# Optimization experiments

Hardware: AMD Instinct MI355X
Metric: run time of the kernel (lower is better)

## Reference

```python
import jax, jax.numpy as jnp
import numpy as np

NX = 41                      # cube side: 2*r_max/voxel + 1 with r_max=6.0, voxel=0.3
VOXEL = 0.3
R_MAX = 6.0
MIN_DIST = 0.8
MIN_SEP = max(1, int(round(MIN_DIST / VOXEL)))   # 3 voxels
K = 4                        # topk_per_channel
NEG = -1.0e9                 # fp32 sentinel used by the torch module
VALID_THRESH = -1.0e8


def setup_inputs() -> dict:
    key = jax.random.key(0)
    B, N, C = 1, 128, 4
    G = NX ** 3
    ax = np.arange(NX)
    ii, jj, kk = np.meshgrid(ax, ax, ax, indexing='ij')
    coords = np.stack([ii, jj, kk], axis=-1).reshape(-1, 3)          # [G,3] integer voxel coords
    center = (NX - 1) / 2.0
    grid_xyz = ((coords - center) * VOXEL).astype(np.float32)        # [G,3] local Angstrom coords
    sphere_mask = np.linalg.norm(grid_xyz, axis=-1) <= R_MAX         # [G] bool
    k1, k2, k3 = jax.random.split(key, 3)
    density = jax.random.normal(k1, (B, N, C, G), jnp.float32)
    A = jax.random.normal(k2, (B, N, 3, 3), jnp.float32)
    Rmats, _ = jnp.linalg.qr(A)                                      # proper-ish rotation matrices
    tpos = jax.random.normal(k3, (B, N, 3), jnp.float32)
    node_mask = jnp.ones((B, N), jnp.float32)
    return dict(density=density,
                grid_xyz=jnp.asarray(grid_xyz),
                sphere_mask=jnp.asarray(sphere_mask),
                coords_int=jnp.asarray(coords, jnp.int32),
                Rmats=Rmats, tpos=tpos, node_mask=node_mask)


def extract_peaks(density, grid_xyz, sphere_mask, coords_int):
    # density: [B,N,C,G]; iterative argmax peak-picking with Chebyshev NMS suppression.
    v0 = jnp.where(sphere_mask[None, None, None, :], density, NEG)
    cx = coords_int[:, 0][None, None, None, :]   # [1,1,1,G]
    cy = coords_int[:, 1][None, None, None, :]
    cz = coords_int[:, 2][None, None, None, :]

    def step(v, _):
        idx = jnp.argmax(v, axis=-1)                                   # [B,N,C]
        score = jnp.take_along_axis(v, idx[..., None], axis=-1)[..., 0]
        valid = score > VALID_THRESH
        xyz = grid_xyz[idx]                                            # [B,N,C,3]
        ijk = coords_int[idx]                                          # [B,N,C,3]
        # Chebyshev (max-abs) voxel distance to the picked peak, per axis to avoid a [.,G,3] temp
        d = jnp.maximum(jnp.maximum(jnp.abs(cx - ijk[..., 0:1]),
                                    jnp.abs(cy - ijk[..., 1:2])),
                        jnp.abs(cz - ijk[..., 2:3]))                    # [B,N,C,G]
        suppress = (d <= MIN_SEP) & valid[..., None]
        v = jnp.where(suppress, NEG, v)
        out = (jnp.where(valid, score, NEG),
               jnp.where(valid[..., None], xyz, 0.0),
               valid)
        return v, out

    _, (scores, xyz, mask) = jax.lax.scan(step, v0, None, length=K)
    # K is leading scan axis -> move to axis 3 giving [B,N,C,K,...]
    return (jnp.moveaxis(xyz, 0, 3), jnp.moveaxis(scores, 0, 3), jnp.moveaxis(mask, 0, 3))


def reference(density, grid_xyz, sphere_mask, coords_int, Rmats, tpos, node_mask):
    peaks_xyz, peaks_score, peaks_mask = extract_peaks(density, grid_xyz, sphere_mask, coords_int)
    # local -> global frame: R @ x + t
    coords_global = jnp.einsum('bnij,bnckj->bncki', Rmats, peaks_xyz) + tpos[:, :, None, None, :]
    m = node_mask[..., None, None, None]                                # [B,N,1,1,1]
    coords_local = peaks_xyz * m
    coords_global = coords_global * m
    scores = peaks_score * node_mask[..., None, None]
    mask = peaks_mask & node_mask.astype(bool)[..., None, None]
    return coords_local, coords_global, scores, mask
```

## Files before the change

kernel.cpp:

```cpp
#include <hip/hip_runtime.h>

#define G_VOX  68921
#define GMAX   68920
#define NSEG   272
#define MWORDS 2176
#define NEGV (-1.0e9f)
#define VTH  (-1.0e8f)

__device__ __forceinline__ bool sphere_bit(const float* __restrict__ gxyz, int e) {
    if (e >= G_VOX) return false;
    float gx = gxyz[e * 3 + 0];
    float gy = gxyz[e * 3 + 1];
    float gz = gxyz[e * 3 + 2];
    float s  = __fadd_rn(__fadd_rn(__fmul_rn(gx, gx), __fmul_rn(gy, gy)),
                         __fmul_rn(gz, gz));
    return (__fsqrt_rn(s) <= 6.0f);
}

__global__ __launch_bounds__(256) void build_mask(
    const float* __restrict__ gxyz, unsigned int* __restrict__ mask)
{
    int idx = blockIdx.x * 256 + threadIdx.x;
    unsigned long long bal = __ballot(sphere_bit(gxyz, idx));
    int lane = threadIdx.x & 63;
    if (lane == 0)       mask[idx >> 5] = (unsigned int)bal;
    else if (lane == 32) mask[idx >> 5] = (unsigned int)(bal >> 32);
}

__device__ __forceinline__ void seg_scan8_core(
    const float* __restrict__ dens, const unsigned int* smw,
    int ebase, int sh, int eclamp, float& bv, int& bi)
{
    bv = NEGV; bi = ebase;
    float4       dq[8];
    unsigned int bq[8];
    unsigned int wprev = smw[0];
    #pragma unroll
    for (int q = 0; q < 8; ++q) {
        const int e = ebase + 32 * q;
        const unsigned int wnext = smw[q + 1];
        unsigned long long mw = ((unsigned long long)wnext << 32) | wprev;
        bq[q] = (unsigned int)(mw >> sh) & 0xFu;
        wprev = wnext;
        const int ec = (e + 3 <= GMAX) ? e : eclamp;
        if (bq[q]) dq[q] = *reinterpret_cast<const float4*>(dens + ec);
    }
    #pragma unroll
    for (int q = 0; q < 8; ++q) {
        if (bq[q]) {
            const int e = ebase + 32 * q;
            float v0 = (bq[q] & 1u) ? dq[q].x : NEGV;
            float v1 = (bq[q] & 2u) ? dq[q].y : NEGV;
            float v2 = (bq[q] & 4u) ? dq[q].z : NEGV;
            float v3 = (bq[q] & 8u) ? dq[q].w : NEGV;
            if (v0 > bv) { bv = v0; bi = e;     }
            if (v1 > bv) { bv = v1; bi = e + 1; }
            if (v2 > bv) { bv = v2; bi = e + 2; }
            if (v3 > bv) { bv = v3; bi = e + 3; }
        }
    }
    #pragma unroll
    for (int off = 4; off > 0; off >>= 1) {
        float ov = __shfl_xor(bv, off);
        int   oi = __shfl_xor(bi, off);
        if (ov > bv || (ov == bv && oi < bi)) { bv = ov; bi = oi; }
    }
}

__global__ __launch_bounds__(512) void fused_peaks(
    const float* __restrict__ density,
    const float* __restrict__ gxyz,
    const unsigned int* __restrict__ maskg,
    const float* __restrict__ Rm, const float* __restrict__ tp,
    const float* __restrict__ nmask,
    float* __restrict__ out)
{
    __shared__ unsigned int smask[MWORDS + 2];
    __shared__ float sval[NSEG];
    __shared__ int   sidx[NSEG];
    __shared__ int   flag[NSEG];
    __shared__ int   list[104];
    __shared__ int   nlist;
    __shared__ float rv[8];
    __shared__ int   ri[8];
    __shared__ float pval[4];
    __shared__ int   pidx[4];
    __shared__ int   pki[4], pkj[4], pkk[4];

    const int tid  = threadIdx.x;
    const int nc   = blockIdx.x;
    const int n    = nc >> 2;
    const int h    = (-nc) & 3;
    const int lane = tid & 63;
    const int w    = tid >> 6;
    const int s8   = lane >> 3;
    const int l8   = lane & 7;
    const float* dens = density + (size_t)nc * G_VOX;
    const int eclamp = h + ((GMAX - 3 - h) & ~3);

    for (int i = tid; i < MWORDS + 2; i += 512) smask[i] = (i < MWORDS) ? maskg[i] : 0u;
    for (int i = tid; i < NSEG; i += 512) flag[i] = 0;
    __syncthreads();

    for (int g = w; g < 34; g += 8) {
        const int s = g * 8 + s8;
        const int ebase = h + 256 * s + 4 * l8;
        float bv; int bi;
        seg_scan8_core(dens, smask + 8 * s, ebase, h + 4 * l8, eclamp, bv, bi);
        if (l8 == 0) { sval[s] = bv; sidx[s] = bi; }
    }
    __syncthreads();

    for (int p = 0; p < 4; ++p) {
        float bv = -INFINITY;
        int   bi = 0x7FFFFFFF;
        if (tid < NSEG) { bv = sval[tid]; bi = sidx[tid]; }
        #pragma unroll
        for (int off = 32; off > 0; off >>= 1) {
            float ov = __shfl_down(bv, off);
            int   oi = __shfl_down(bi, off);
            if (ov > bv || (ov == bv && oi < bi)) { bv = ov; bi = oi; }
        }
        if (lane == 0) { rv[w] = bv; ri[w] = bi; }
        __syncthreads();
        if (w == 0) {
            bv = (lane < 8) ? rv[lane] : -INFINITY;
            bi = (lane < 8) ? ri[lane] : 0x7FFFFFFF;
            #pragma unroll
            for (int off = 4; off > 0; off >>= 1) {
                float ov = __shfl_down(bv, off);
                int   oi = __shfl_down(bi, off);
                if (ov > bv || (ov == bv && oi < bi)) { bv = ov; bi = oi; }
            }
            if (lane == 0) {
                pval[p] = bv;
                pidx[p] = bi;
                int pi = bi / 1681;
                int rr = bi - pi * 1681;
                int pj = rr / 41;
                pki[p] = pi; pkj[p] = pj; pkk[p] = rr - pj * 41;
                nlist = 0;
            }
        }
        __syncthreads();

        if (p < 3 && pval[p] > VTH) {
            if (tid < 49) {
                int di = tid / 7 - 3, dj = tid % 7 - 3;
                int ii = pki[p] + di, jj = pkj[p] + dj;
                if (ii >= 0 && ii <= 40 && jj >= 0 && jj <= 40) {
                    int k0 = pkk[p] - 3; if (k0 < 0)  k0 = 0;
                    int k1 = pkk[p] + 3; if (k1 > 40) k1 = 40;
                    int b0  = ii * 1681 + jj * 41 + k0;
                    int cnt = k1 - k0 + 1;
                    unsigned long long m = ((1ull << cnt) - 1ull) << (b0 & 31);
                    int w0 = b0 >> 5;
                    atomicAnd(&smask[w0], ~(unsigned int)m);
                    unsigned int hi = (unsigned int)(m >> 32);
                    if (hi) atomicAnd(&smask[w0 + 1], ~hi);
                    int s0 = (b0 > h) ? (b0 - h) >> 8 : 0;
                    int s1 = (b0 + cnt - 1 > h) ? (b0 + cnt - 1 - h) >> 8 : 0;
                    #pragma unroll
                    for (int t2 = 0; t2 < 2; ++t2) {
                        const int s = t2 ? s1 : s0;
                        if (t2 && s1 == s0) break;
                        int widx = sidx[s];
                        int wi = widx / 1681;
                        int wr = widx - wi * 1681;
                        int wj = wr / 41;
                        int wk = wr - wj * 41;
                        int ci = wi - pki[p]; if (ci < 0) ci = -ci;
                        int cj = wj - pkj[p]; if (cj < 0) cj = -cj;
                        int ck = wk - pkk[p]; if (ck < 0) ck = -ck;
                        if (ci <= 3 && cj <= 3 && ck <= 3) {
                            if (atomicMax(&flag[s], p + 1) < p + 1) {
                                int q = atomicAdd(&nlist, 1); list[q] = s;
                            }
                        }
                    }
                }
            }
            __syncthreads();
            const int cnt = nlist;
            for (int base = 0; base < cnt; base += 64) {
                const int slot = base + w * 8 + s8;
                if (slot < cnt) {
                    const int s = list[slot];
                    const int ebase = h + 256 * s + 4 * l8;
                    float bv2; int bi2;
                    seg_scan8_core(dens, smask + 8 * s, ebase, h + 4 * l8, eclamp, bv2, bi2);
                    if (l8 == 0) { sval[s] = bv2; sidx[s] = bi2; }
                }
            }
        }
        __syncthreads();
    }

    if (tid < 4) {
        const int k   = tid;
        const float val = pval[k];
        const int   idx = pidx[k];
        const bool valid = val > VTH;
        float gx = 0.0f, gy = 0.0f, gz = 0.0f;
        if (valid) {
            gx = gxyz[idx * 3 + 0];
            gy = gxyz[idx * 3 + 1];
            gz = gxyz[idx * 3 + 2];
        }
        const float nm = nmask[n];
        const float* R = Rm + n * 9;
        const float* t = tp + n * 3;
        float wx = R[0] * gx + R[1] * gy + R[2] * gz + t[0];
        float wy = R[3] * gx + R[4] * gy + R[5] * gz + t[1];
        float wz = R[6] * gx + R[7] * gy + R[8] * gz + t[2];

        const size_t o3 = ((size_t)nc * 4 + k) * 3;
        out[o3 + 0] = gx * nm;
        out[o3 + 1] = gy * nm;
        out[o3 + 2] = gz * nm;
        out[6144 + o3 + 0] = wx * nm;
        out[6144 + o3 + 1] = wy * nm;
        out[6144 + o3 + 2] = wz * nm;
        const size_t o1 = (size_t)nc * 4 + k;
        out[12288 + o1] = (valid ? val : NEGV) * nm;
        out[14336 + o1] = (valid && nm != 0.0f) ? 1.0f : 0.0f;
    }
}

extern "C" void kernel_launch(void* const* d_in, const int* in_sizes, int n_in,
                              void* d_out, int out_size, void* d_ws, size_t ws_size,
                              hipStream_t stream) {
    const float* density  = (const float*)d_in[0];
    const float* grid_xyz = (const float*)d_in[1];
    const float* Rm    = (const float*)d_in[4];
    const float* tpos  = (const float*)d_in[5];
    const float* nmask = (const float*)d_in[6];
    float* out = (float*)d_out;

    unsigned int* mask = (unsigned int*)d_ws;

    build_mask<<<dim3(272), dim3(256), 0, stream>>>(grid_xyz, mask);
    fused_peaks<<<dim3(512), dim3(512), 0, stream>>>(density, grid_xyz, mask,
                                                     Rm, tpos, nmask, out);
}
```

Before: 221.9 us.

## Run iterative peak-pick and NMS rescans in a single wavefront without block barriers

After the initial full segment scan, the four peak-pick iterations (argmax reduction, mask suppression, and rescans of affected segments) now run entirely in wavefront 0. Block-wide __syncthreads and the cross-wave shared-memory reduction are dropped in favour of wave-level shuffles. The aim is to cut barrier and reduction latency in the serial tail. In exchange, the rescans of affected segments use 8 lanes-groups of one wave instead of all 8 waves, so rescan throughput drops. Correctness also now depends on lockstep execution within the wave for the LDS atomics and the list reads.

Result: no change. 218.7 us (-1.4%).

```diff
diff --git a/kernel.cpp b/kernel.cpp
--- a/kernel.cpp
+++ b/kernel.cpp
@@ -81,11 +81,8 @@
     __shared__ int   flag[NSEG];
     __shared__ int   list[104];
     __shared__ int   nlist;
-    __shared__ float rv[8];
-    __shared__ int   ri[8];
     __shared__ float pval[4];
     __shared__ int   pidx[4];
-    __shared__ int   pki[4], pkj[4], pkk[4];
 
     const int tid  = threadIdx.x;
     const int nc   = blockIdx.x;
@@ -111,119 +108,107 @@
     }
     __syncthreads();
 
-    for (int p = 0; p < 4; ++p) {
-        float bv = -INFINITY;
-        int   bi = 0x7FFFFFFF;
-        if (tid < NSEG) { bv = sval[tid]; bi = sidx[tid]; }
-        #pragma unroll
-        for (int off = 32; off > 0; off >>= 1) {
-            float ov = __shfl_down(bv, off);
-            int   oi = __shfl_down(bi, off);
-            if (ov > bv || (ov == bv && oi < bi)) { bv = ov; bi = oi; }
-        }
-        if (lane == 0) { rv[w] = bv; ri[w] = bi; }
-        __syncthreads();
-        if (w == 0) {
-            bv = (lane < 8) ? rv[lane] : -INFINITY;
-            bi = (lane < 8) ? ri[lane] : 0x7FFFFFFF;
+    if (w == 0) {
+        for (int p = 0; p < 4; ++p) {
+            float bv = -INFINITY;
+            int   bi = 0x7FFFFFFF;
+            for (int t = lane; t < NSEG; t += 64) {
+                float v = sval[t]; int ix = sidx[t];
+                if (v > bv || (v == bv && ix < bi)) { bv = v; bi = ix; }
+            }
             #pragma unroll
-            for (int off = 4; off > 0; off >>= 1) {
+            for (int off = 32; off > 0; off >>= 1) {
                 float ov = __shfl_down(bv, off);
                 int   oi = __shfl_down(bi, off);
                 if (ov > bv || (ov == bv && oi < bi)) { bv = ov; bi = oi; }
             }
-            if (lane == 0) {
-                pval[p] = bv;
-                pidx[p] = bi;
-                int pi = bi / 1681;
-                int rr = bi - pi * 1681;
-                int pj = rr / 41;
-                pki[p] = pi; pkj[p] = pj; pkk[p] = rr - pj * 41;
-                nlist = 0;
-            }
-        }
-        __syncthreads();
-
-        if (p < 3 && pval[p] > VTH) {
-            if (tid < 49) {
-                int di = tid / 7 - 3, dj = tid % 7 - 3;
-                int ii = pki[p] + di, jj = pkj[p] + dj;
-                if (ii >= 0 && ii <= 40 && jj >= 0 && jj <= 40) {
-                    int k0 = pkk[p] - 3; if (k0 < 0)  k0 = 0;
-                    int k1 = pkk[p] + 3; if (k1 > 40) k1 = 40;
-                    int b0  = ii * 1681 + jj * 41 + k0;
-                    int cnt = k1 - k0 + 1;
-                    unsigned long long m = ((1ull << cnt) - 1ull) << (b0 & 31);
-                    int w0 = b0 >> 5;
-                    atomicAnd(&smask[w0], ~(unsigned int)m);
-                    unsigned int hi = (unsigned int)(m >> 32);
-                    if (hi) atomicAnd(&smask[w0 + 1], ~hi);
-                    int s0 = (b0 > h) ? (b0 - h) >> 8 : 0;
-                    int s1 = (b0 + cnt - 1 > h) ? (b0 + cnt - 1 - h) >> 8 : 0;
-                    #pragma unroll
-                    for (int t2 = 0; t2 < 2; ++t2) {
-                        const int s = t2 ? s1 : s0;
-                        if (t2 && s1 == s0) break;
-                        int widx = sidx[s];
-                        int wi = widx / 1681;
-                        int wr = widx - wi * 1681;
-                        int wj = wr / 41;
-                        int wk = wr - wj * 41;
-                        int ci = wi - pki[p]; if (ci < 0) ci = -ci;
-                        int cj = wj - pkj[p]; if (cj < 0) cj = -cj;
-                        int ck = wk - pkk[p]; if (ck < 0) ck = -ck;
-                        if (ci <= 3 && cj <= 3 && ck <= 3) {
-                            if (atomicMax(&flag[s], p + 1) < p + 1) {
-                                int q = atomicAdd(&nlist, 1); list[q] = s;
+            const float pv = __shfl(bv, 0);
+            const int   px = __shfl(bi, 0);
+            if (lane == 0) { pval[p] = pv; pidx[p] = px; nlist = 0; }
+            const int pi = px / 1681;
+            const int rr = px - pi * 1681;
+            const int pj = rr / 41;
+            const int pk = rr - pj * 41;
+
+            if (p < 3 && pv > VTH) {
+                if (lane < 49) {
+                    int di = lane / 7 - 3, dj = lane % 7 - 3;
+                    int ii = pi + di, jj = pj + dj;
+                    if (ii >= 0 && ii <= 40 && jj >= 0 && jj <= 40) {
+                        int k0 = pk - 3; if (k0 < 0)  k0 = 0;
+                        int k1 = pk + 3; if (k1 > 40) k1 = 40;
+                        int b0  = ii * 1681 + jj * 41 + k0;
+                        int cnt = k1 - k0 + 1;
+                        unsigned long long m = ((1ull << cnt) - 1ull) << (b0 & 31);
+                        int w0 = b0 >> 5;
+                        atomicAnd(&smask[w0], ~(unsigned int)m);
+                        unsigned int hi = (unsigned int)(m >> 32);
+                        if (hi) atomicAnd(&smask[w0 + 1], ~hi);
+                        int s0 = (b0 > h) ? (b0 - h) >> 8 : 0;
+                        int s1 = (b0 + cnt - 1 > h) ? (b0 + cnt - 1 - h) >> 8 : 0;
+                        #pragma unroll
+                        for (int t2 = 0; t2 < 2; ++t2) {
+                            const int s = t2 ? s1 : s0;
+                            if (t2 && s1 == s0) break;
+                            int widx = sidx[s];
+                            int wi = widx / 1681;
+                            int wr = widx - wi * 1681;
+                            int wj = wr / 41;
+                            int wk = wr - wj * 41;
+                            int ci = wi - pi; if (ci < 0) ci = -ci;
+                            int cj = wj - pj; if (cj < 0) cj = -cj;
+                            int ck = wk - pk; if (ck < 0) ck = -ck;
+                            if (ci <= 3 && cj <= 3 && ck <= 3) {
+                                if (atomicMax(&flag[s], p + 1) < p + 1) {
+                                    int q = atomicAdd(&nlist, 1); list[q] = s;
+                                }
                             }
                         }
                     }
                 }
-            }
-            __syncthreads();
-            const int cnt = nlist;
-            for (int base = 0; base < cnt; base += 64) {
-                const int slot = base + w * 8 + s8;
-                if (slot < cnt) {
-                    const int s = list[slot];
-                    const int ebase = h + 256 * s + 4 * l8;
-                    float bv2; int bi2;
-                    seg_scan8_core(dens, smask + 8 * s, ebase, h + 4 * l8, eclamp, bv2, bi2);
-                    if (l8 == 0) { sval[s] = bv2; sidx[s] = bi2; }
+                const int cnt = nlist;
+                for (int base = 0; base < cnt; base += 8) {
+                    const int slot = base + s8;
+                    if (slot < cnt) {
+                        const int s = list[slot];
+                        const int ebase = h + 256 * s + 4 * l8;
+                        float bv2; int bi2;
+                        seg_scan8_core(dens, smask + 8 * s, ebase, h + 4 * l8, eclamp, bv2, bi2);
+                        if (l8 == 0) { sval[s] = bv2; sidx[s] = bi2; }
+                    }
                 }
             }
         }
-        __syncthreads();
-    }
-
-    if (tid < 4) {
-        const int k   = tid;
-        const float val = pval[k];
-        const int   idx = pidx[k];
-        const bool valid = val > VTH;
-        float gx = 0.0f, gy = 0.0f, gz = 0.0f;
-        if (valid) {
-            gx = gxyz[idx * 3 + 0];
-            gy = gxyz[idx * 3 + 1];
-            gz = gxyz[idx * 3 + 2];
+
+        if (lane < 4) {
+            const int k   = lane;
+            const float val = pval[k];
+            const int   idx = pidx[k];
+            const bool valid = val > VTH;
+            float gx = 0.0f, gy = 0.0f, gz = 0.0f;
+            if (valid) {
+                gx = gxyz[idx * 3 + 0];
+                gy = gxyz[idx * 3 + 1];
+                gz = gxyz[idx * 3 + 2];
+            }
+            const float nm = nmask[n];
+            const float* R = Rm + n * 9;
+            const float* t = tp + n * 3;
+            float wx = R[0] * gx + R[1] * gy + R[2] * gz + t[0];
+            float wy = R[3] * gx + R[4] * gy + R[5] * gz + t[1];
+            float wz = R[6] * gx + R[7] * gy + R[8] * gz + t[2];
+
+            const size_t o3 = ((size_t)nc * 4 + k) * 3;
+            out[o3 + 0] = gx * nm;
+            out[o3 + 1] = gy * nm;
+            out[o3 + 2] = gz * nm;
+            out[6144 + o3 + 0] = wx * nm;
+            out[6144 + o3 + 1] = wy * nm;
+            out[6144 + o3 + 2] = wz * nm;
+            const size_t o1 = (size_t)nc * 4 + k;
+            out[12288 + o1] = (valid ? val : NEGV) * nm;
+            out[14336 + o1] = (valid && nm != 0.0f) ? 1.0f : 0.0f;
         }
-        const float nm = nmask[n];
-        const float* R = Rm + n * 9;
-        const float* t = tp + n * 3;
-        float wx = R[0] * gx + R[1] * gy + R[2] * gz + t[0];
-        float wy = R[3] * gx + R[4] * gy + R[5] * gz + t[1];
-        float wz = R[6] * gx + R[7] * gy + R[8] * gz + t[2];
-
-        const size_t o3 = ((size_t)nc * 4 + k) * 3;
-        out[o3 + 0] = gx * nm;
-        out[o3 + 1] = gy * nm;
-        out[o3 + 2] = gz * nm;
-        out[6144 + o3 + 0] = wx * nm;
-        out[6144 + o3 + 1] = wy * nm;
-        out[6144 + o3 + 2] = wz * nm;
-        const size_t o1 = (size_t)nc * 4 + k;
-        out[12288 + o1] = (valid ? val : NEGV) * nm;
-        out[14336 + o1] = (valid && nm != 0.0f) ? 1.0f : 0.0f;
     }
 }
 
```
